# Optimization experiments

Measured on AMD Instinct MI355X. Metric: run time of the kernel, lower is better.

Reference implementation:

```python
import jax, jax.numpy as jnp
import numpy as np
import math

B, L, H, E, D = 4, 1024, 8, 64, 64
T_STEPS = 1000


def setup_inputs() -> dict:
    key = jax.random.key(0)
    ks = jax.random.split(key, 6)
    queries = jax.random.normal(ks[0], (B, L, H, E), dtype=jnp.float32)
    keys = jax.random.normal(ks[1], (B, L, H, E), dtype=jnp.float32)
    values = jax.random.normal(ks[2], (B, L, H, D), dtype=jnp.float32)
    sigma = jax.random.normal(ks[3], (B, L, H), dtype=jnp.float32)
    sqrt_alphas_cumprod = jax.random.uniform(ks[4], (T_STEPS,), dtype=jnp.float32)
    t = jax.random.randint(ks[5], (B,), 0, T_STEPS)
    return {
        "queries": queries,
        "keys": keys,
        "values": values,
        "sigma": sigma,
        "sqrt_alphas_cumprod": sqrt_alphas_cumprod,
        "t": t,
    }


def reference(queries, keys, values, sigma, sqrt_alphas_cumprod, t):
    B_, L_, H_, E_ = queries.shape
    scale = 1.0 / math.sqrt(E_)

    # scores: [B,H,L,S]
    scores = jnp.einsum("blhe,bshe->bhls", queries, keys)
    # causal mask (triu, diagonal=1) -> -inf, then scale (mask_flag=True, attn_mask=None)
    causal = jnp.triu(jnp.ones((L_, L_), dtype=bool), k=1)
    attn = scale * jnp.where(causal, -jnp.inf, scores)

    # sigma pipeline: [B,L,H] -> [B,H,L] -> nonlinear chain
    sg = jnp.transpose(sigma, (0, 2, 1))               # [B,H,L]
    sg = jax.nn.sigmoid(sg * 5.0) + 1e-5
    sg = jnp.power(3.0, sg) - 1.0                      # in (0, 2)

    # per-batch diffusion scale: sqrt_alphas_cumprod[t] -> [B,1,1]
    sac_t = sqrt_alphas_cumprod[t][:, None, None]      # [B,1,1]
    sigma_t = jnp.broadcast_to((sac_t * sg)[..., None], (B_, H_, L_, L_))

    # |i-j| distance matrix, Gaussian prior
    idx = jnp.arange(L_)
    dist = jnp.abs(idx[:, None] - idx[None, :]).astype(jnp.float32)  # [L,L]
    inv_sqrt_2pi = 1.0 / math.sqrt(2.0 * math.pi)
    prior = inv_sqrt_2pi / sigma_t * jnp.exp(-(dist ** 2) / 2.0 / (sigma_t ** 2))

    series = jax.nn.softmax(attn, axis=-1)             # dropout p=0.0
    V = jnp.einsum("bhls,bshd->blhd", series, values)
    return V, series, prior, sigma_t
```

## Files before the change

kernel.cpp:

```cpp
#include <hip/hip_runtime.h>
#include <hip/hip_bf16.h>
#include <cstddef>
#include <cstdint>

namespace {

using f32x4  = __attribute__((ext_vector_type(4))) float;
using bf16x8 = __attribute__((ext_vector_type(8))) short;
using u16x4  = __attribute__((ext_vector_type(4))) unsigned short;

constexpr int TOTAL_BLOCKS = 5120;
constexpr int PSTR = 1032;

__device__ inline unsigned short f2bf(float x) {
  __hip_bfloat16 hv = __float2bfloat16(x);
  return *reinterpret_cast<unsigned short*>(&hv);
}
__device__ inline float bf2f(unsigned short u) {
  return __uint_as_float(((unsigned int)u) << 16);
}
__device__ inline bf16x8 pack_bf8(f32x4 a, f32x4 b) {
  bf16x8 r;
  r[0] = (short)f2bf(a[0]); r[1] = (short)f2bf(a[1]);
  r[2] = (short)f2bf(a[2]); r[3] = (short)f2bf(a[3]);
  r[4] = (short)f2bf(b[0]); r[5] = (short)f2bf(b[1]);
  r[6] = (short)f2bf(b[2]); r[7] = (short)f2bf(b[3]);
  return r;
}
__device__ inline bf16x8 pack8(const float* p) {
  bf16x8 r;
#pragma unroll
  for (int i = 0; i < 8; ++i) r[i] = (short)f2bf(p[i]);
  return r;
}

__global__ __launch_bounds__(256) void fused_all(
    const float* __restrict__ Qg, const float* __restrict__ Kg,
    const float* __restrict__ Vg, const float* __restrict__ Sg,
    const float* __restrict__ sacg, const int* __restrict__ tg,
    float* __restrict__ outV, float* __restrict__ outS,
    float* __restrict__ outP, float* __restrict__ outT)
{
  __shared__ unsigned short Pl[32 * PSTR];
  __shared__ float red[4][32];
  __shared__ float invl[32];

  const int tid = threadIdx.x;
  const int bid = blockIdx.x;
  const int role5 = bid / 5;

  if (bid - role5 * 5 != 0) {
    const int pb = role5 * 4 + (bid - role5 * 5) - 1;
    const int ln = tid & 63;
    const float sac = sacg[tg[(pb * 8) >> 13]];
#pragma unroll
    for (int rr = 0; rr < 2; ++rr) {
      const int r0 = pb * 8 + rr * 4 + (tid >> 6);
      const int b  = r0 >> 13;
      const int hh = (r0 >> 10) & 7;
      const int l  = r0 & 1023;
      const float sgv = Sg[(size_t)(b * 1024 + l) * 8 + hh];
      const float sig = 1.f / (1.f + __expf(-5.f * sgv)) + 1e-5f;
      const float st  = sac * expm1f(sig * 1.0986122886681098f);
      const float coef = 0.3989422804014327f / st;
      const float qc   = -0.5f / (st * st);
      float* pp = outP + ((size_t)r0 << 10);
      float* tp = outT + ((size_t)r0 << 10);
      const f32x4 stv = {st, st, st, st};
#pragma unroll
      for (int j = 0; j < 4; ++j) {
        const int c0 = j * 256 + ln * 4;
        const float d0 = (float)(l - c0);
        const float d1 = d0 - 1.f, d2 = d0 - 2.f, d3 = d0 - 3.f;
        f32x4 pr;
        pr[0] = coef * __expf(qc * d0 * d0);
        pr[1] = coef * __expf(qc * d1 * d1);
        pr[2] = coef * __expf(qc * d2 * d2);
        pr[3] = coef * __expf(qc * d3 * d3);
        __builtin_nontemporal_store(pr, reinterpret_cast<f32x4*>(pp + c0));
        __builtin_nontemporal_store(stv, reinterpret_cast<f32x4*>(tp + c0));
      }
    }
    return;
  }

  const int aid = role5;
  const int w = tid >> 6, ln = tid & 63;
  const int g = ln >> 4, n16 = ln & 15;
  const int bh = aid & 31, b = bh >> 3, h = bh & 7;
  const int qt = 31 - (aid >> 5);
  const int qb = qt * 32;
  const int nch = (qt >> 1) + 1;

  const float* Qbase = Qg + ((size_t)(b * 1024) * 8 + h) * 64;
  const float* Kbase = Kg + ((size_t)(b * 1024) * 8 + h) * 64;
  const float* Vbase = Vg + ((size_t)(b * 1024) * 8 + h) * 64;

  bf16x8 qf[2][2];
#pragma unroll
  for (int u = 0; u < 2; ++u) {
    const float* qr = Qbase + (size_t)(qb + u * 16 + n16) * 512 + 8 * g;
    qf[u][0] = pack_bf8(*(const f32x4*)(qr),      *(const f32x4*)(qr + 4));
    qf[u][1] = pack_bf8(*(const f32x4*)(qr + 32), *(const f32x4*)(qr + 36));
  }

  f32x4 O[2] = {};
  float cs[2] = {0.f, 0.f};

  const float* vcol = Vbase + (size_t)(8 * g) * 512 + w * 16 + n16;

  float vrA[16], vrB[16];
  auto vload = [&](int c, float (&dst)[16]) {
    const float* p = vcol + (size_t)c * 64 * 512;
#pragma unroll
    for (int h2 = 0; h2 < 2; ++h2)
#pragma unroll
      for (int j = 0; j < 8; ++j)
        dst[h2 * 8 + j] = p[(size_t)(32 * h2 + j) * 512];
  };

  auto body = [&](int c, float (&vc)[16], float (&vn)[16]) {
    const float* kr = Kbase + (size_t)(c * 64 + w * 16 + n16) * 512 + 8 * g;
    const bf16x8 kf0 = pack_bf8(*(const f32x4*)(kr),      *(const f32x4*)(kr + 4));
    const bf16x8 kf1 = pack_bf8(*(const f32x4*)(kr + 32), *(const f32x4*)(kr + 36));

#pragma unroll
    for (int u = 0; u < 2; ++u) {
      f32x4 acc = {0.f, 0.f, 0.f, 0.f};
      acc = __builtin_amdgcn_mfma_f32_16x16x32_bf16(kf0, qf[u][0], acc, 0, 0, 0);
      acc = __builtin_amdgcn_mfma_f32_16x16x32_bf16(kf1, qf[u][1], acc, 0, 0, 0);
      const int qlane = qb + u * 16 + n16;
      const int sbase = c * 64 + w * 16 + 4 * g;
      const float e0 = (sbase + 0 <= qlane) ? __expf(acc[0] * 0.125f) : 0.f;
      const float e1 = (sbase + 1 <= qlane) ? __expf(acc[1] * 0.125f) : 0.f;
      const float e2 = (sbase + 2 <= qlane) ? __expf(acc[2] * 0.125f) : 0.f;
      const float e3 = (sbase + 3 <= qlane) ? __expf(acc[3] * 0.125f) : 0.f;
      cs[u] += (e0 + e1) + (e2 + e3);
      u16x4 pk = {f2bf(e0), f2bf(e1), f2bf(e2), f2bf(e3)};
      *reinterpret_cast<u16x4*>(&Pl[(u * 16 + n16) * PSTR + sbase]) = pk;
    }

    if (c + 1 < nch) vload(c + 1, vn);

    __syncthreads();

    const bf16x8 vv0 = pack8(&vc[0]);
    const bf16x8 vv1 = pack8(&vc[8]);
#pragma unroll
    for (int u = 0; u < 2; ++u) {
      const bf16x8 pa0 =
          *reinterpret_cast<const bf16x8*>(&Pl[(u * 16 + n16) * PSTR + c * 64 + 8 * g]);
      O[u] = __builtin_amdgcn_mfma_f32_16x16x32_bf16(pa0, vv0, O[u], 0, 0, 0);
      const bf16x8 pa1 =
          *reinterpret_cast<const bf16x8*>(&Pl[(u * 16 + n16) * PSTR + c * 64 + 32 + 8 * g]);
      O[u] = __builtin_amdgcn_mfma_f32_16x16x32_bf16(pa1, vv1, O[u], 0, 0, 0);
    }
  };

  vload(0, vrA);
  int c = 0;
  while (true) {
    body(c, vrA, vrB);
    if (++c >= nch) break;
    body(c, vrB, vrA);
    if (++c >= nch) break;
  }

  cs[0] += __shfl_xor(cs[0], 16); cs[0] += __shfl_xor(cs[0], 32);
  cs[1] += __shfl_xor(cs[1], 16); cs[1] += __shfl_xor(cs[1], 32);
  if (ln < 16) { red[w][n16] = cs[0]; red[w][16 + n16] = cs[1]; }
  __syncthreads();
  if (tid < 32) {
    const float s = red[0][tid] + red[1][tid] + red[2][tid] + red[3][tid];
    invl[tid] = 1.f / s;
  }
  __syncthreads();

  {
    float* Vo = outV + ((size_t)(b * 1024) * 8 + h) * 64;
#pragma unroll
    for (int u = 0; u < 2; ++u)
#pragma unroll
      for (int r = 0; r < 4; ++r) {
        const int qrow = u * 16 + 4 * g + r;
        __builtin_nontemporal_store(O[u][r] * invl[qrow],
                                    Vo + (size_t)(qb + qrow) * 512 + w * 16 + n16);
      }
  }

  {
    const int r = tid >> 3, sub = tid & 7;
    float* Srow = outS + ((size_t)bh * 1024 + qb + r) * 1024;
    const float il = invl[r];
    const int slim = nch * 64;
#pragma unroll 4
    for (int j = 0; j < 32; ++j) {
      const int s = j * 32 + sub * 4;
      f32x4 o;
      if (s < slim) {
        const u16x4 p = *reinterpret_cast<const u16x4*>(&Pl[r * PSTR + s]);
        o[0] = bf2f(p[0]) * il;
        o[1] = bf2f(p[1]) * il;
        o[2] = bf2f(p[2]) * il;
        o[3] = bf2f(p[3]) * il;
      } else {
        o = (f32x4){0.f, 0.f, 0.f, 0.f};
      }
      __builtin_nontemporal_store(o, reinterpret_cast<f32x4*>(Srow + s));
    }
  }
}

}

extern "C" void kernel_launch(void* const* d_in, const int* in_sizes, int n_in,
                              void* d_out, int out_size, void* d_ws, size_t ws_size,
                              hipStream_t stream) {
  const float* Qg   = (const float*)d_in[0];
  const float* Kg   = (const float*)d_in[1];
  const float* Vg   = (const float*)d_in[2];
  const float* Sg   = (const float*)d_in[3];
  const float* sacg = (const float*)d_in[4];
  const int*   tg   = (const int*)d_in[5];

  float* out  = (float*)d_out;
  float* outV = out;
  float* outS = out + (size_t)2097152;
  float* outP = out + (size_t)35651584;
  float* outT = out + (size_t)69206016;

  hipLaunchKernelGGL(fused_all, dim3(TOTAL_BLOCKS), dim3(256), 0, stream,
                     Qg, Kg, Vg, Sg, sacg, tg, outV, outS, outP, outT);
}
```

Measured before the change: 81.63 us.

## Move masked series zero-fill from attention blocks to prior blocks

Attention blocks now write only the causal part of their series rows. The zero-filled upper-triangle tiles are written by the prior/sigma blocks, which each compute a triangular index mapping to two 32x64 zero tiles. This is meant to shift store work off the heavier attention blocks and balance bandwidth use across the grid. The prior blocks also batch their exp computations before issuing the grouped non-temporal stores. The cost is extra integer and sqrt index math per prior block, and correctness depends on that mapping covering each masked tile exactly once.

```diff
diff --git a/kernel.cpp b/kernel.cpp
--- a/kernel.cpp
+++ b/kernel.cpp
@@ -67,18 +67,43 @@
       float* pp = outP + ((size_t)r0 << 10);
       float* tp = outT + ((size_t)r0 << 10);
       const f32x4 stv = {st, st, st, st};
+      f32x4 prj[4];
 #pragma unroll
       for (int j = 0; j < 4; ++j) {
         const int c0 = j * 256 + ln * 4;
         const float d0 = (float)(l - c0);
         const float d1 = d0 - 1.f, d2 = d0 - 2.f, d3 = d0 - 3.f;
-        f32x4 pr;
-        pr[0] = coef * __expf(qc * d0 * d0);
-        pr[1] = coef * __expf(qc * d1 * d1);
-        pr[2] = coef * __expf(qc * d2 * d2);
-        pr[3] = coef * __expf(qc * d3 * d3);
-        __builtin_nontemporal_store(pr, reinterpret_cast<f32x4*>(pp + c0));
-        __builtin_nontemporal_store(stv, reinterpret_cast<f32x4*>(tp + c0));
+        prj[j][0] = coef * __expf(qc * d0 * d0);
+        prj[j][1] = coef * __expf(qc * d1 * d1);
+        prj[j][2] = coef * __expf(qc * d2 * d2);
+        prj[j][3] = coef * __expf(qc * d3 * d3);
+      }
+#pragma unroll
+      for (int j = 0; j < 4; ++j)
+        __builtin_nontemporal_store(prj[j], reinterpret_cast<f32x4*>(pp + j * 256 + ln * 4));
+#pragma unroll
+      for (int j = 0; j < 4; ++j)
+        __builtin_nontemporal_store(stv, reinterpret_cast<f32x4*>(tp + j * 256 + ln * 4));
+    }
+
+    if (pb < 3840) {
+      const f32x4 z4 = {0.f, 0.f, 0.f, 0.f};
+#pragma unroll
+      for (int zz = 0; zz < 2; ++zz) {
+        const int z  = pb * 2 + zz;
+        const int bh = z / 240;
+        const int r  = z - bh * 240;
+        int i = (int)((31.0f - sqrtf((float)(961 - 4 * r))) * 0.5f);
+        if (i > 0 && i * (31 - i) > r) --i;
+        if ((i + 1) * (30 - i) <= r) ++i;
+        const int off = r - i * (31 - i);
+        const int w15 = 15 - i;
+        const int qt  = 2 * i + (off >= w15 ? 1 : 0);
+        const int c   = (i + 1) + (off >= w15 ? off - w15 : off);
+        const int row = tid >> 3;
+        float* p = outS + (((size_t)bh * 1024 + qt * 32 + row) << 10) + c * 64 + (tid & 7) * 8;
+        __builtin_nontemporal_store(z4, reinterpret_cast<f32x4*>(p));
+        __builtin_nontemporal_store(z4, reinterpret_cast<f32x4*>(p + 4));
       }
     }
     return;
@@ -192,20 +217,16 @@
     const int r = tid >> 3, sub = tid & 7;
     float* Srow = outS + ((size_t)bh * 1024 + qb + r) * 1024;
     const float il = invl[r];
-    const int slim = nch * 64;
+    const int jmax = nch << 1;
 #pragma unroll 4
-    for (int j = 0; j < 32; ++j) {
+    for (int j = 0; j < jmax; ++j) {
       const int s = j * 32 + sub * 4;
+      const u16x4 p = *reinterpret_cast<const u16x4*>(&Pl[r * PSTR + s]);
       f32x4 o;
-      if (s < slim) {
-        const u16x4 p = *reinterpret_cast<const u16x4*>(&Pl[r * PSTR + s]);
-        o[0] = bf2f(p[0]) * il;
-        o[1] = bf2f(p[1]) * il;
-        o[2] = bf2f(p[2]) * il;
-        o[3] = bf2f(p[3]) * il;
-      } else {
-        o = (f32x4){0.f, 0.f, 0.f, 0.f};
-      }
+      o[0] = bf2f(p[0]) * il;
+      o[1] = bf2f(p[1]) * il;
+      o[2] = bf2f(p[2]) * il;
+      o[3] = bf2f(p[3]) * il;
       __builtin_nontemporal_store(o, reinterpret_cast<f32x4*>(Srow + s));
     }
   }
```

Result: slower. 93.70 us (+14.8%).
